# Optimization experiments

Measured on AMD Instinct MI355X. Metric: run time of the kernel, lower is better.

The kernel has to match this reference:

```python
import jax, jax.numpy as jnp
import numpy as np

GRID_SIZE = 3
SPLINE_ORDER = 3
GRID_RANGE = (-1.0, 1.0)


def make_grid():
    # extended knot vector, shape (1, grid_size + 2*spline_order + 1) = (1, 10)
    h = (GRID_RANGE[1] - GRID_RANGE[0]) / GRID_SIZE
    pts = np.arange(-SPLINE_ORDER, GRID_SIZE + SPLINE_ORDER + 1, dtype=np.float32) * h + GRID_RANGE[0]
    return jnp.asarray(pts[None, :])  # broadcasts over in_features


def b_splines(x, grid):
    # x: (B, in) -> bases: (B, in, grid_size + spline_order)
    x = x[..., None]  # (B, in, 1)
    bases = ((x >= grid[:, :-1]) & (x < grid[:, 1:])).astype(x.dtype)
    for k in range(1, SPLINE_ORDER + 1):
        left = (x - grid[:, : -(k + 1)]) / (grid[:, k:-1] - grid[:, : -(k + 1)])
        right = (grid[:, k + 1:] - x) / (grid[:, k + 1:] - grid[:, 1:-k])
        bases = left * bases[..., :-1] + right * bases[..., 1:]
    return bases


def kan_linear(x, base_w, spline_w, scaler, grid):
    # efficient-kan KANLinear: silu(x)@base_w.T + b_splines(x) contracted with scaled spline weights
    base_out = jnp.einsum('bi,oi->bo', jax.nn.silu(x), base_w)
    bases = b_splines(x, grid)  # (B, in, 6)
    spline_out = jnp.einsum('bik,oik->bo', bases, spline_w * scaler[..., None])
    return base_out + spline_out


def layer_norm(x, gamma, beta, eps=1e-5):
    mu = jnp.mean(x, axis=-1, keepdims=True)
    var = jnp.mean(jnp.square(x - mu), axis=-1, keepdims=True)
    return (x - mu) * jax.lax.rsqrt(var + eps) * gamma + beta


def setup_inputs() -> dict:
    key = jax.random.key(0)
    ks = jax.random.split(key, 8)
    B, D_IN, D_HID, D_OUT = 16384, 1280, 512, 229
    NB = GRID_SIZE + SPLINE_ORDER  # 6 basis functions per input feature
    s1 = 1.0 / np.sqrt(D_IN)
    s2 = 1.0 / np.sqrt(D_HID)
    return {
        'x': jax.random.normal(ks[0], (B, D_IN), dtype=jnp.float32),
        'base_w1': jax.random.normal(ks[1], (D_HID, D_IN), dtype=jnp.float32) * s1,
        'spline_w1': jax.random.normal(ks[2], (D_HID, D_IN, NB), dtype=jnp.float32) * s1,
        'scaler1': jax.random.normal(ks[3], (D_HID, D_IN), dtype=jnp.float32) * 0.1 + 1.0,
        'ln_gamma': jnp.ones((D_HID,), dtype=jnp.float32),
        'ln_beta': jnp.zeros((D_HID,), dtype=jnp.float32),
        'base_w2': jax.random.normal(ks[4], (D_OUT, D_HID), dtype=jnp.float32) * s2,
        'spline_w2': jax.random.normal(ks[5], (D_OUT, D_HID, NB), dtype=jnp.float32) * s2,
        'scaler2': jax.random.normal(ks[6], (D_OUT, D_HID), dtype=jnp.float32) * 0.1 + 1.0,
    }


def reference(x, base_w1, spline_w1, scaler1, ln_gamma, ln_beta, base_w2, spline_w2, scaler2):
    grid = make_grid()
    h = kan_linear(x, base_w1, spline_w1, scaler1, grid)   # (B, 512)
    h = layer_norm(h, ln_gamma, ln_beta)                    # dropout: identity at inference
    out = kan_linear(h, base_w2, spline_w2, scaler2, grid)  # (B, 229)
    return out
```

## Files before the change

### kernel.cpp

```cpp
#include <hip/hip_runtime.h>


typedef short s16x8 __attribute__((ext_vector_type(8)));
typedef float f32x4 __attribute__((ext_vector_type(4)));

__device__ __forceinline__ void dma16(const void* g, void* l) {
  __builtin_amdgcn_global_load_lds(
      (const __attribute__((address_space(1))) unsigned int*)g,
      (__attribute__((address_space(3))) unsigned int*)l, 16, 0, 0);
}

__device__ __forceinline__ unsigned pk2(float lo, float hi) {
  unsigned a = __float_as_uint(lo), b = __float_as_uint(hi);
  a = a + 0x7fffu + ((a >> 16) & 1u);
  b = b + 0x7fffu + ((b >> 16) & 1u);
  return __builtin_amdgcn_perm(b, a, 0x07060302u);
}

__device__ __forceinline__ unsigned short f2bf(float f) {
  unsigned u = __float_as_uint(f);
  unsigned r = u + 0x7fffu + ((u >> 16) & 1u);
  return (unsigned short)(r >> 16);
}

__device__ __forceinline__ uint4 kan_act8(float x) {
  float e = __expf(-x);
  float s = x * __builtin_amdgcn_rcpf(1.0f + e);
  float u = fmaf(x, 1.5f, 4.5f);
  float d[10];
#pragma unroll
  for (int j = 0; j < 10; ++j) d[j] = u - (float)j;
  float b1[8];
#pragma unroll
  for (int j = 0; j < 8; ++j) b1[j] = fmaxf(0.0f, 1.0f - fabsf(d[j + 1]));
  float B2[7];
#pragma unroll
  for (int j = 0; j < 7; ++j) B2[j] = d[j] * b1[j] - d[j + 3] * b1[j + 1];
  float b3[6];
#pragma unroll
  for (int j = 0; j < 6; ++j)
    b3[j] = (d[j] * B2[j] - d[j + 4] * B2[j + 1]) * (1.0f / 6.0f);
  uint4 r;
  r.x = pk2(s, b3[0]);
  r.y = pk2(b3[1], b3[2]);
  r.z = pk2(b3[3], b3[4]);
  r.w = pk2(b3[5], 0.0f);
  return r;
}

__global__ __launch_bounds__(256) void prep_w(
    const float* __restrict__ base_w, const float* __restrict__ spline_w,
    const float* __restrict__ scaler, short* __restrict__ Wp,
    int F, int Nvalid) {
  int i = blockIdx.x * 256 + threadIdx.x;
  int n = blockIdx.y;
  if (i >= F) return;
  s16x8 v;
#pragma unroll
  for (int k = 0; k < 8; ++k) v[k] = 0;
  if (n < Nvalid) {
    int idx = n * F + i;
    float sc = scaler[idx];
    v[0] = (short)f2bf(base_w[idx]);
#pragma unroll
    for (int k = 0; k < 6; ++k) v[1 + k] = (short)f2bf(spline_w[idx * 6 + k] * sc);
  }
  int p = (i & ~3) | ((i & 3) ^ (n & 3));
  *(s16x8*)&Wp[((size_t)n * F + p) * 8] = v;
}

template <int BN>
__global__ __launch_bounds__(512, 2) void kan_gemm(
    const float* __restrict__ X, const short* __restrict__ W,
    float* __restrict__ Cp, int F, int span, long long pstride,
    int ldc, int ncols) {
  constexpr int NT = BN / 64;
  constexpr int IE = BN / 128;
  __shared__ __align__(16) short As[2][128 * 32];
  __shared__ __align__(16) short Bs[2][BN * 32];

  const int t    = threadIdx.x;
  const int lane = t & 63;
  const int w    = t >> 6;
  const int m0   = blockIdx.x * 128;
  const int f0   = blockIdx.z * span;

  const int wrow = (w >> 2) * 64;
  const int wcol = (w & 3) * (BN / 4);
  const int mrow = lane & 15;
  const int q    = lane >> 4;
  const int qs   = (q ^ (mrow & 3)) * 8;

  int a_off[4], b_off[NT];
#pragma unroll
  for (int it = 0; it < 4; ++it)
    a_off[it] = (wrow + it * 16 + mrow) * 32 + qs;
#pragma unroll
  for (int jt = 0; jt < NT; ++jt)
    b_off[jt] = (wcol + jt * 16 + mrow) * 32 + qs;

  const int sr = t >> 2, sj = t & 3;
  const float* xq = X + (size_t)(m0 + sr) * F + f0 + sj;
  const int aw = sr * 32 + ((sj ^ (sr & 3)) * 8);

  const int drow = w * (BN / 8) + (lane >> 2);
  const int dchk = lane & 3;
  const char* wg = (const char*)W + ((size_t)drow * F + f0) * 16 +
                   (size_t)dchk * 16;
  const size_t gistr = (size_t)16 * F * 16;

  f32x4 acc[4][NT] = {};
  const int nsteps = span >> 2;

  {
    float xv = *xq;
#pragma unroll
    for (int e = 0; e < IE; ++e)
      dma16(wg + e * gistr, &Bs[0][(w * (BN / 8) + e * 16) * 32]);
    uint4 av = kan_act8(xv);
    *(uint4*)&As[0][aw] = av;
  }
  __syncthreads();

  for (int ks = 0; ks < nsteps; ++ks) {
    const int cb = ks & 1, nb = cb ^ 1;
    const bool more = (ks + 1 < nsteps);
    float xn = 0.0f;
    if (more) {
#pragma unroll
      for (int e = 0; e < IE; ++e)
        dma16(wg + (size_t)(ks + 1) * 64 + e * gistr,
              &Bs[nb][(w * (BN / 8) + e * 16) * 32]);
      xn = xq[(size_t)(ks + 1) * 4];
    }

    s16x8 af[4], bfr[NT];
#pragma unroll
    for (int it = 0; it < 4; ++it)
      af[it] = *(const s16x8*)&As[cb][a_off[it]];
#pragma unroll
    for (int jt = 0; jt < NT; ++jt)
      bfr[jt] = *(const s16x8*)&Bs[cb][b_off[jt]];
#pragma unroll
    for (int a = 0; a < 4; ++a)
#pragma unroll
      for (int b = 0; b < NT; ++b)
        acc[a][b] = __builtin_amdgcn_mfma_f32_16x16x32_bf16(
            af[a], bfr[b], acc[a][b], 0, 0, 0);

    if (more) {
      uint4 av = kan_act8(xn);
      *(uint4*)&As[nb][aw] = av;
    }
    __syncthreads();
  }

  float* cpt = Cp + (size_t)blockIdx.z * (size_t)pstride;
#pragma unroll
  for (int a = 0; a < 4; ++a) {
#pragma unroll
    for (int b = 0; b < NT; ++b) {
      int col = wcol + b * 16 + mrow;
      if (col < ncols) {
#pragma unroll
        for (int r = 0; r < 4; ++r) {
          int row = m0 + wrow + a * 16 + q * 4 + r;
          cpt[(size_t)row * ldc + col] = acc[a][b][r];
        }
      }
    }
  }
}

__global__ __launch_bounds__(256) void ln_reduce(
    const float* __restrict__ p0, const float* __restrict__ p1,
    float* __restrict__ h, const float* __restrict__ gamma,
    const float* __restrict__ beta, int nparts) {
  int lane = threadIdx.x & 63;
  int wv   = threadIdx.x >> 6;
  int row  = blockIdx.x * 4 + wv;
  size_t base = (size_t)row * 512 + lane * 8;
  f32x4 v0 = *(const f32x4*)(p0 + base);
  f32x4 v1 = *(const f32x4*)(p0 + base + 4);
  if (nparts == 2) {
    f32x4 u0 = *(const f32x4*)(p1 + base);
    f32x4 u1 = *(const f32x4*)(p1 + base + 4);
#pragma unroll
    for (int k = 0; k < 4; ++k) { v0[k] += u0[k]; v1[k] += u1[k]; }
  }
  float s = 0.f, s2 = 0.f;
#pragma unroll
  for (int k = 0; k < 4; ++k) { s += v0[k] + v1[k]; s2 += v0[k]*v0[k] + v1[k]*v1[k]; }
#pragma unroll
  for (int m = 32; m >= 1; m >>= 1) {
    s  += __shfl_xor(s,  m, 64);
    s2 += __shfl_xor(s2, m, 64);
  }
  float mean = s * (1.0f / 512.0f);
  float var  = s2 * (1.0f / 512.0f) - mean * mean;
  float rstd = rsqrtf(var + 1e-5f);
  const f32x4 g0 = *(const f32x4*)(gamma + lane * 8);
  const f32x4 g1 = *(const f32x4*)(gamma + lane * 8 + 4);
  const f32x4 be0 = *(const f32x4*)(beta + lane * 8);
  const f32x4 be1 = *(const f32x4*)(beta + lane * 8 + 4);
#pragma unroll
  for (int k = 0; k < 4; ++k) {
    v0[k] = (v0[k] - mean) * rstd * g0[k] + be0[k];
    v1[k] = (v1[k] - mean) * rstd * g1[k] + be1[k];
  }
  *(f32x4*)(h + base) = v0;
  *(f32x4*)(h + base + 4) = v1;
}

__global__ __launch_bounds__(256) void out_reduce(
    const float* __restrict__ p0, const float* __restrict__ p1,
    float* __restrict__ out, int nparts) {
  int idx = blockIdx.x * 256 + threadIdx.x;
  int row = idx >> 8;
  int c   = idx & 255;
  float v = p0[idx];
  if (nparts == 2) v += p1[idx];
  if (c < 229) out[(size_t)row * 229 + c] = v;
}

extern "C" void kernel_launch(void* const* d_in, const int* in_sizes, int n_in,
                              void* d_out, int out_size, void* d_ws, size_t ws_size,
                              hipStream_t stream) {
  const float* x         = (const float*)d_in[0];
  const float* base_w1   = (const float*)d_in[1];
  const float* spline_w1 = (const float*)d_in[2];
  const float* scaler1   = (const float*)d_in[3];
  const float* ln_gamma  = (const float*)d_in[4];
  const float* ln_beta   = (const float*)d_in[5];
  const float* base_w2   = (const float*)d_in[6];
  const float* spline_w2 = (const float*)d_in[7];
  const float* scaler2   = (const float*)d_in[8];
  float* out = (float*)d_out;

  const int B = 16384, D_IN = 1280, D_HID = 512, D_OUT = 229;

  const size_t szW1 = (size_t)D_HID * D_IN * 8 * 2;
  const size_t szW2 = (size_t)256 * D_HID * 8 * 2;
  const size_t szH  = (size_t)B * D_HID * 4;
  const size_t szP  = (size_t)B * 512 * 4;
  char* ws = (char*)d_ws;
  short* W1p = (short*)ws;
  short* W2p = (short*)(ws + szW1);
  float* h   = (float*)(ws + szW1 + szW2);
  float* p0  = (float*)(ws + szW1 + szW2 + szH);
  float* p1  = (float*)(ws + szW1 + szW2 + szH + szP);

  const int parts = (ws_size >= szW1 + szW2 + szH + 2 * szP) ? 2 : 1;
  const long long pstride = (long long)(szP / 4);

  prep_w<<<dim3(D_IN / 256, D_HID), 256, 0, stream>>>(
      base_w1, spline_w1, scaler1, W1p, D_IN, D_HID);
  prep_w<<<dim3(D_HID / 256, 256), 256, 0, stream>>>(
      base_w2, spline_w2, scaler2, W2p, D_HID, D_OUT);

  kan_gemm<512><<<dim3(B / 128, 1, parts), 512, 0, stream>>>(
      x, W1p, p0, D_IN, D_IN / parts, pstride, D_HID, D_HID);

  ln_reduce<<<dim3(B / 4), 256, 0, stream>>>(p0, p1, h, ln_gamma, ln_beta, parts);

  kan_gemm<256><<<dim3(B / 128, 1, parts), 512, 0, stream>>>(
      h, W2p, p0, D_HID, D_HID / parts, pstride, 256, 256);

  out_reduce<<<dim3(B * 256 / 256), 256, 0, stream>>>(p0, p1, out, parts);
}
```

Baseline: 466.4 us.

## Load weight fragments directly from global memory instead of staging in LDS

The weight tile is no longer copied into shared memory with async global-to-LDS loads. Each wave now reads its B fragments straight from global memory (through L2/L1), and the XOR swizzle in the weight prep is dropped. The x prefetch is moved one step further ahead, and the MFMA loop order is swapped. This cuts LDS traffic and LDS capacity, which may allow more occupancy. In exchange, weight loads are no longer shared across the two row-waves, so global/L2 traffic goes up and load latency sits on the critical path with no double buffering.

```diff
diff --git a/kernel.cpp b/kernel.cpp
--- a/kernel.cpp
+++ b/kernel.cpp
@@ -3,12 +3,6 @@
 
 typedef short s16x8 __attribute__((ext_vector_type(8)));
 typedef float f32x4 __attribute__((ext_vector_type(4)));
-
-__device__ __forceinline__ void dma16(const void* g, void* l) {
-  __builtin_amdgcn_global_load_lds(
-      (const __attribute__((address_space(1))) unsigned int*)g,
-      (__attribute__((address_space(3))) unsigned int*)l, 16, 0, 0);
-}
 
 __device__ __forceinline__ unsigned pk2(float lo, float hi) {
   unsigned a = __float_as_uint(lo), b = __float_as_uint(hi);
@@ -65,8 +59,7 @@
 #pragma unroll
     for (int k = 0; k < 6; ++k) v[1 + k] = (short)f2bf(spline_w[idx * 6 + k] * sc);
   }
-  int p = (i & ~3) | ((i & 3) ^ (n & 3));
-  *(s16x8*)&Wp[((size_t)n * F + p) * 8] = v;
+  *(s16x8*)&Wp[((size_t)n * F + i) * 8] = v;
 }
 
 template <int BN>
@@ -75,15 +68,14 @@
     float* __restrict__ Cp, int F, int span, long long pstride,
     int ldc, int ncols) {
   constexpr int NT = BN / 64;
-  constexpr int IE = BN / 128;
   __shared__ __align__(16) short As[2][128 * 32];
-  __shared__ __align__(16) short Bs[2][BN * 32];
 
   const int t    = threadIdx.x;
   const int lane = t & 63;
   const int w    = t >> 6;
   const int m0   = blockIdx.x * 128;
   const int f0   = blockIdx.z * span;
+  const size_t K8 = (size_t)F * 8;
 
   const int wrow = (w >> 2) * 64;
   const int wcol = (w & 3) * (BN / 4);
@@ -91,66 +83,53 @@
   const int q    = lane >> 4;
   const int qs   = (q ^ (mrow & 3)) * 8;
 
-  int a_off[4], b_off[NT];
+  int a_off[4];
 #pragma unroll
   for (int it = 0; it < 4; ++it)
     a_off[it] = (wrow + it * 16 + mrow) * 32 + qs;
-#pragma unroll
-  for (int jt = 0; jt < NT; ++jt)
-    b_off[jt] = (wcol + jt * 16 + mrow) * 32 + qs;
+
+  const short* wb0 = W + (size_t)(wcol + mrow) * K8 + (size_t)(f0 + q) * 8;
+  const size_t jstr = 16 * K8;
 
   const int sr = t >> 2, sj = t & 3;
   const float* xq = X + (size_t)(m0 + sr) * F + f0 + sj;
   const int aw = sr * 32 + ((sj ^ (sr & 3)) * 8);
 
-  const int drow = w * (BN / 8) + (lane >> 2);
-  const int dchk = lane & 3;
-  const char* wg = (const char*)W + ((size_t)drow * F + f0) * 16 +
-                   (size_t)dchk * 16;
-  const size_t gistr = (size_t)16 * F * 16;
-
   f32x4 acc[4][NT] = {};
   const int nsteps = span >> 2;
 
+  float xn = *xq;
   {
-    float xv = *xq;
-#pragma unroll
-    for (int e = 0; e < IE; ++e)
-      dma16(wg + e * gistr, &Bs[0][(w * (BN / 8) + e * 16) * 32]);
-    uint4 av = kan_act8(xv);
+    uint4 av = kan_act8(xn);
     *(uint4*)&As[0][aw] = av;
   }
+  if (nsteps > 1) xn = xq[4];
   __syncthreads();
 
   for (int ks = 0; ks < nsteps; ++ks) {
     const int cb = ks & 1, nb = cb ^ 1;
-    const bool more = (ks + 1 < nsteps);
-    float xn = 0.0f;
-    if (more) {
-#pragma unroll
-      for (int e = 0; e < IE; ++e)
-        dma16(wg + (size_t)(ks + 1) * 64 + e * gistr,
-              &Bs[nb][(w * (BN / 8) + e * 16) * 32]);
-      xn = xq[(size_t)(ks + 1) * 4];
-    }
-
-    s16x8 af[4], bfr[NT];
+
+    s16x8 bfr[NT];
+#pragma unroll
+    for (int jt = 0; jt < NT; ++jt)
+      bfr[jt] = *(const s16x8*)(wb0 + jt * jstr + (size_t)ks * 32);
+
+    s16x8 af[4];
 #pragma unroll
     for (int it = 0; it < 4; ++it)
       af[it] = *(const s16x8*)&As[cb][a_off[it]];
-#pragma unroll
-    for (int jt = 0; jt < NT; ++jt)
-      bfr[jt] = *(const s16x8*)&Bs[cb][b_off[jt]];
-#pragma unroll
-    for (int a = 0; a < 4; ++a)
-#pragma unroll
-      for (int b = 0; b < NT; ++b)
+
+#pragma unroll
+    for (int b = 0; b < NT; ++b)
+#pragma unroll
+      for (int a = 0; a < 4; ++a)
         acc[a][b] = __builtin_amdgcn_mfma_f32_16x16x32_bf16(
             af[a], bfr[b], acc[a][b], 0, 0, 0);
 
-    if (more) {
+    if (ks + 1 < nsteps) {
       uint4 av = kan_act8(xn);
       *(uint4*)&As[nb][aw] = av;
+      if (ks + 2 < nsteps) xn = xq[(size_t)(ks + 2) * 4];
     }
     __syncthreads();
   }
```

Result: slower. 689.7 us (+47.9%).
